# Kernel tuning notes

Measured on AMD Instinct MI355X. Metric: run time of the kernel, lower is better.

The kernel has to match this reference:

```python
import jax, jax.numpy as jnp
import numpy as np

DIM = 16
HEADS = 2
EPS = 1e-5


def _layer_norm(x, g, b):
    m = x.mean(-1, keepdims=True)
    v = ((x - m) ** 2).mean(-1, keepdims=True)
    return (x - m) * jax.lax.rsqrt(v + EPS) * g + b


def setup_inputs() -> dict:
    key = jax.random.key(0)
    ks = jax.random.split(key, 8)
    B, Lq, Lk, D = 4, 2048, 2048, DIM
    xavier = float(np.sqrt(6.0 / (D + D)))  # xavier_uniform bound for square Linear
    inp = {
        "query": jax.random.normal(ks[0], (B, Lq, D), jnp.float32),
        "key": jax.random.normal(ks[1], (B, Lk, D), jnp.float32),
        "value": jax.random.normal(ks[2], (B, Lk, D), jnp.float32),
        "w": jax.random.normal(ks[3], (B, HEADS, Lq, Lk), jnp.float32) * 0.1,
        "mask": jnp.zeros((B, HEADS, Lq, Lk), jnp.float32),
        # LayerNorm params (q, k, v)
        "ln_qg": jnp.ones((D,), jnp.float32), "ln_qb": jnp.zeros((D,), jnp.float32),
        "ln_kg": jnp.ones((D,), jnp.float32), "ln_kb": jnp.zeros((D,), jnp.float32),
        "ln_vg": jnp.ones((D,), jnp.float32), "ln_vb": jnp.zeros((D,), jnp.float32),
        # Linear projections, torch layout [out, in]
        "Wq": jax.random.uniform(ks[4], (D, D), jnp.float32, -xavier, xavier),
        "bq": jnp.zeros((D,), jnp.float32),
        "Wk": jax.random.uniform(ks[5], (D, D), jnp.float32, -xavier, xavier),
        "bk": jnp.zeros((D,), jnp.float32),
        "Wv": jax.random.uniform(ks[6], (D, D), jnp.float32, -xavier, xavier),
        "bv": jnp.zeros((D,), jnp.float32),
        "Wo": jax.random.normal(ks[7], (D, D), jnp.float32) * (1.0 / np.sqrt(D)),
        "bo": jnp.zeros((D,), jnp.float32),
    }
    return inp


def reference(query, key, value, w, mask,
              ln_qg, ln_qb, ln_kg, ln_kb, ln_vg, ln_vb,
              Wq, bq, Wk, bk, Wv, bv, Wo, bo):
    B, Lq, D = query.shape
    H = HEADS
    dh = D // H
    q = _layer_norm(query, ln_qg, ln_qb)
    k = _layer_norm(key, ln_kg, ln_kb)
    v = _layer_norm(value, ln_vg, ln_vb)
    q0 = q  # residual is post-LayerNorm query
    # torch Linear: x @ W.T + b ; split heads -> [B, H, L, dh]
    Q = (q @ Wq.T + bq).reshape(B, Lq, H, dh).transpose(0, 2, 1, 3)
    K = (k @ Wk.T + bk).reshape(B, -1, H, dh).transpose(0, 2, 1, 3)
    V = (v @ Wv.T + bv).reshape(B, -1, H, dh).transpose(0, 2, 1, 3)
    Q = Q / (dh ** 0.5)
    scores = jnp.einsum('bhqd,bhkd->bhqk', Q, K) + w
    scores = scores - scores.max(axis=-1, keepdims=True)
    scores = scores + mask
    attn = jax.nn.softmax(scores, axis=-1)  # dropout is identity in eval
    ctx = jnp.einsum('bhqk,bhkd->bhqd', attn, V)
    ctx = ctx.transpose(0, 2, 1, 3).reshape(B, Lq, D)
    out = ctx @ Wo.T + bo + q0
    return out, attn
```

## Files before the change

### kernel.cpp

```cpp
#include <hip/hip_runtime.h>
#include <math.h>

#define BATCH 4
#define LQ 2048
#define LK 2048
#define DIM 16
#define HEADS 2
#define DH 8
#define EPS 1e-5f

typedef float fvec4 __attribute__((ext_vector_type(4)));
typedef unsigned int uvec4 __attribute__((ext_vector_type(4)));
typedef unsigned int uvec2 __attribute__((ext_vector_type(2)));
typedef __fp16 hvec2 __attribute__((ext_vector_type(2)));

__device__ __forceinline__ hvec2 u2h(unsigned u) {
    union { unsigned u; hvec2 h; } c; c.u = u; return c.h;
}
__device__ __forceinline__ unsigned h2u(hvec2 h) {
    union { unsigned u; hvec2 h; } c; c.h = h; return c.u;
}

__global__ __launch_bounds__(256) void ln_proj3_kernel(
    const float* __restrict__ xq, const float* __restrict__ xk,
    const float* __restrict__ xv,
    const float* __restrict__ gq, const float* __restrict__ bq_ln,
    const float* __restrict__ gk, const float* __restrict__ bk_ln,
    const float* __restrict__ gv, const float* __restrict__ bv_ln,
    const float* __restrict__ Wq, const float* __restrict__ bq,
    const float* __restrict__ Wk, const float* __restrict__ bk,
    const float* __restrict__ Wv, const float* __restrict__ bv,
    float* __restrict__ Qb, unsigned* __restrict__ Kh,
    unsigned short* __restrict__ Vh, float* __restrict__ q0)
{
    const int gid = blockIdx.x * blockDim.x + threadIdx.x;
    const int which = gid >> 13;
    const int r     = gid & 8191;

    const float* x; const float* g; const float* bl;
    const float* W; const float* bb; float scale;
    if (which == 0)      { x = xq; g = gq; bl = bq_ln; W = Wq; bb = bq; scale = 0.35355339059327373f; }
    else if (which == 1) { x = xk; g = gk; bl = bk_ln; W = Wk; bb = bk; scale = 1.0f; }
    else                 { x = xv; g = gv; bl = bv_ln; W = Wv; bb = bv; scale = 1.0f; }

    float xv16[16];
    const float4* xp = (const float4*)(x + (size_t)r * 16);
#pragma unroll
    for (int i = 0; i < 4; ++i) {
        float4 t = xp[i];
        xv16[4*i+0] = t.x; xv16[4*i+1] = t.y; xv16[4*i+2] = t.z; xv16[4*i+3] = t.w;
    }
    float m = 0.f;
#pragma unroll
    for (int i = 0; i < 16; ++i) m += xv16[i];
    m *= (1.f / 16.f);
    float var = 0.f;
#pragma unroll
    for (int i = 0; i < 16; ++i) { float d = xv16[i] - m; var += d * d; }
    var *= (1.f / 16.f);
    float rs = rsqrtf(var + EPS);

    float xn[16];
#pragma unroll
    for (int i = 0; i < 16; ++i) xn[i] = (xv16[i] - m) * rs * g[i] + bl[i];

    if (which == 0) {
        float4* op = (float4*)(q0 + (size_t)r * 16);
#pragma unroll
        for (int i = 0; i < 4; ++i) {
            float4 t; t.x = xn[4*i+0]; t.y = xn[4*i+1]; t.z = xn[4*i+2]; t.w = xn[4*i+3];
            op[i] = t;
        }
    }

    float pr[16];
#pragma unroll
    for (int j = 0; j < 16; ++j) {
        float acc = bb[j];
#pragma unroll
        for (int i = 0; i < 16; ++i) acc += xn[i] * W[j * 16 + i];
        pr[j] = acc * scale;
    }

    const int b = r >> 11;
    const int l = r & 2047;
    if (which == 0) {
#pragma unroll
        for (int j = 0; j < 16; ++j) {
            int h = j >> 3, d = j & 7;
            Qb[((((size_t)b * HEADS + h) * 2048) + l) * DH + d] = pr[j];
        }
    } else if (which == 1) {
#pragma unroll
        for (int h = 0; h < 2; ++h) {
            unsigned* Kpan = Kh + ((size_t)(b * 2 + h)) * 8192;
#pragma unroll
            for (int p = 0; p < 4; ++p) {
                hvec2 hk = __builtin_amdgcn_cvt_pkrtz(pr[h * 8 + 2 * p], pr[h * 8 + 2 * p + 1]);
                Kpan[p * 2048 + l] = h2u(hk);
            }
        }
    } else {
#pragma unroll
        for (int h = 0; h < 2; ++h) {
            unsigned short* Vpan = Vh + ((size_t)(b * 2 + h)) * 16384;
#pragma unroll
            for (int d = 0; d < 8; ++d) {
                union { __fp16 h; unsigned short u; } cv;
                cv.h = (__fp16)pr[h * 8 + d];
                Vpan[d * 2048 + l] = cv.u;
            }
        }
    }
}

__device__ __forceinline__ float wave_sum(float v) {
#pragma unroll
    for (int off = 32; off > 0; off >>= 1) v += __shfl_xor(v, off);
    return v;
}

__global__ __launch_bounds__(256, 2) void attn_kernel(
    const float* __restrict__ Q,
    const unsigned* __restrict__ Kh,
    const unsigned* __restrict__ Vh,
    const float* __restrict__ w,
    const float* __restrict__ mask,
    float* __restrict__ attn_out,
    float* __restrict__ ctx)
{
    __shared__ unsigned Kp[4][2048];
    __shared__ unsigned Vp[8][1024];

    const int t    = threadIdx.x;
    const int lane = t & 63;
    const int wid  = t >> 6;
    const int gr   = (blockIdx.x << 2) + wid;
    const int bh   = gr >> 11;
    const int q    = gr & (LQ - 1);
    const int rowid= gr;
    const int h    = bh & (HEADS - 1);
    const int b    = bh >> 1;

    const unsigned* Kpan = Kh + (size_t)bh * 8192;
    const unsigned* Vpan = Vh + (size_t)bh * 8192;

    {
        const uvec4* Ksrc = (const uvec4*)Kpan;
        const uvec4* Vsrc = (const uvec4*)Vpan;
        uvec4* Kdst = (uvec4*)&Kp[0][0];
        uvec4* Vdst = (uvec4*)&Vp[0][0];
#pragma unroll
        for (int j = 0; j < 8; ++j) {
            Kdst[(j << 8) + t] = Ksrc[(j << 8) + t];
            Vdst[(j << 8) + t] = Vsrc[(j << 8) + t];
        }
    }

    const float* Qrow = Q + (size_t)rowid * DH;
    hvec2 qpk[4];
#pragma unroll
    for (int p = 0; p < 4; ++p) qpk[p] = __builtin_amdgcn_cvt_pkrtz(Qrow[2 * p], Qrow[2 * p + 1]);

    const float* wrow = w    + (size_t)rowid * LK;
    const float* mrow = mask + (size_t)rowid * LK;

    fvec4 wb[8], mb[8];
#pragma unroll
    for (int g = 0; g < 8; ++g) {
        const int col = (g << 8) + (lane << 2);
        wb[g] = __builtin_nontemporal_load((const fvec4*)(wrow + col));
        mb[g] = __builtin_nontemporal_load((const fvec4*)(mrow + col));
    }

    __syncthreads();

    unsigned epk[16];
    float sum = 0.f;
    float cd[8] = {0,0,0,0,0,0,0,0};

#pragma unroll
    for (int i = 0; i < 8; ++i) {
        const fvec4 wv = wb[i], mv = mb[i];
        const int cb = (i << 8) + (lane << 2);
        uvec4 kk0 = *(const uvec4*)&Kp[0][cb];
        uvec4 kk1 = *(const uvec4*)&Kp[1][cb];
        uvec4 kk2 = *(const uvec4*)&Kp[2][cb];
        uvec4 kk3 = *(const uvec4*)&Kp[3][cb];
        float e[4];
#pragma unroll
        for (int j = 0; j < 4; ++j) {
            float sj = wv[j] + mv[j] - 4.0f;
            sj = __builtin_amdgcn_fdot2(qpk[0], u2h(kk0[j]), sj, false);
            sj = __builtin_amdgcn_fdot2(qpk[1], u2h(kk1[j]), sj, false);
            sj = __builtin_amdgcn_fdot2(qpk[2], u2h(kk2[j]), sj, false);
            sj = __builtin_amdgcn_fdot2(qpk[3], u2h(kk3[j]), sj, false);
            e[j] = __expf(sj);
        }
        sum += (e[0] + e[1]) + (e[2] + e[3]);
        hvec2 e01 = __builtin_amdgcn_cvt_pkrtz(e[0], e[1]);
        hvec2 e23 = __builtin_amdgcn_cvt_pkrtz(e[2], e[3]);
        epk[2 * i]     = h2u(e01);
        epk[2 * i + 1] = h2u(e23);
        const int cp = cb >> 1;
#pragma unroll
        for (int d = 0; d < 8; ++d) {
            uvec2 vv = *(const uvec2*)&Vp[d][cp];
            cd[d] = __builtin_amdgcn_fdot2(e01, u2h(vv.x), cd[d], false);
            cd[d] = __builtin_amdgcn_fdot2(e23, u2h(vv.y), cd[d], false);
        }
    }

    sum = wave_sum(sum);
    const float inv = 1.f / sum;

    float* arow = attn_out + (size_t)rowid * LK;
#pragma unroll
    for (int g = 0; g < 8; ++g) {
        const int col = (g << 8) + (lane << 2);
        hvec2 e01 = u2h(epk[2 * g]), e23 = u2h(epk[2 * g + 1]);
        fvec4 o;
        o.x = (float)e01.x * inv; o.y = (float)e01.y * inv;
        o.z = (float)e23.x * inv; o.w = (float)e23.y * inv;
        __builtin_nontemporal_store(o, (fvec4*)(arow + col));
    }

#pragma unroll
    for (int d = 0; d < 8; ++d) cd[d] = wave_sum(cd[d]) * inv;
    if (lane == 0) {
        float* cp = ctx + ((((size_t)b * LQ + q) * HEADS) + h) * DH;
        fvec4 t0; t0.x = cd[0]; t0.y = cd[1]; t0.z = cd[2]; t0.w = cd[3];
        fvec4 t1; t1.x = cd[4]; t1.y = cd[5]; t1.z = cd[6]; t1.w = cd[7];
        ((fvec4*)cp)[0] = t0;
        ((fvec4*)cp)[1] = t1;
    }
}

__global__ __launch_bounds__(256) void out_kernel(
    const float* __restrict__ ctx,
    const float* __restrict__ Wo,
    const float* __restrict__ bo,
    const float* __restrict__ q0,
    float* __restrict__ out, int n)
{
    int gid = blockIdx.x * blockDim.x + threadIdx.x;
    if (gid >= n) return;
    int row = gid >> 4, j = gid & 15;
    const float* c = ctx + (size_t)row * 16;
    float acc = bo[j];
#pragma unroll
    for (int i = 0; i < 16; ++i) acc += c[i] * Wo[j * 16 + i];
    out[gid] = acc + q0[gid];
}

extern "C" void kernel_launch(void* const* d_in, const int* in_sizes, int n_in,
                              void* d_out, int out_size, void* d_ws, size_t ws_size,
                              hipStream_t stream) {
    const float* query = (const float*)d_in[0];
    const float* key_  = (const float*)d_in[1];
    const float* value = (const float*)d_in[2];
    const float* w     = (const float*)d_in[3];
    const float* mask  = (const float*)d_in[4];
    const float* ln_qg = (const float*)d_in[5];
    const float* ln_qb = (const float*)d_in[6];
    const float* ln_kg = (const float*)d_in[7];
    const float* ln_kb = (const float*)d_in[8];
    const float* ln_vg = (const float*)d_in[9];
    const float* ln_vb = (const float*)d_in[10];
    const float* Wq = (const float*)d_in[11];
    const float* bq = (const float*)d_in[12];
    const float* Wk = (const float*)d_in[13];
    const float* bk = (const float*)d_in[14];
    const float* Wv = (const float*)d_in[15];
    const float* bv = (const float*)d_in[16];
    const float* Wo = (const float*)d_in[17];
    const float* bo = (const float*)d_in[18];

    float* out  = (float*)d_out;
    float* attn = out + (size_t)BATCH * LQ * DIM;

    const size_t NE = (size_t)BATCH * LQ * DIM;
    float* ws  = (float*)d_ws;
    float* Qb  = ws;
    float* q0  = Qb + NE;
    float* ctx = q0 + NE;
    unsigned* Kh = (unsigned*)(ctx + NE);
    unsigned short* Vh16 = (unsigned short*)(Kh + 65536);
    unsigned* Vh = (unsigned*)Vh16;

    ln_proj3_kernel<<<(3 * 8192) / 256, 256, 0, stream>>>(
        query, key_, value,
        ln_qg, ln_qb, ln_kg, ln_kb, ln_vg, ln_vb,
        Wq, bq, Wk, bk, Wv, bv,
        Qb, Kh, Vh16, q0);

    attn_kernel<<<BATCH * HEADS * LQ / 4, 256, 0, stream>>>(
        Qb, Kh, Vh, w, mask, attn, ctx);

    out_kernel<<<((int)NE + 255) / 256, 256, 0, stream>>>(
        ctx, Wo, bo, q0, out, (int)NE);
}
```

Measured before the change: 80.91 us.

## Fuse output projection into attention via atomics and stage V from global

```diff
diff --git a/kernel.cpp b/kernel.cpp
--- a/kernel.cpp
+++ b/kernel.cpp
@@ -30,8 +30,10 @@
     const float* __restrict__ Wq, const float* __restrict__ bq,
     const float* __restrict__ Wk, const float* __restrict__ bk,
     const float* __restrict__ Wv, const float* __restrict__ bv,
+    const float* __restrict__ bo,
+    float* __restrict__ outbuf,
     float* __restrict__ Qb, unsigned* __restrict__ Kh,
-    unsigned short* __restrict__ Vh, float* __restrict__ q0)
+    unsigned short* __restrict__ Vh)
 {
     const int gid = blockIdx.x * blockDim.x + threadIdx.x;
     const int which = gid >> 13;
@@ -65,10 +67,12 @@
     for (int i = 0; i < 16; ++i) xn[i] = (xv16[i] - m) * rs * g[i] + bl[i];
 
     if (which == 0) {
-        float4* op = (float4*)(q0 + (size_t)r * 16);
+        float4* op = (float4*)(outbuf + (size_t)r * 16);
 #pragma unroll
         for (int i = 0; i < 4; ++i) {
-            float4 t; t.x = xn[4*i+0]; t.y = xn[4*i+1]; t.z = xn[4*i+2]; t.w = xn[4*i+3];
+            float4 t;
+            t.x = xn[4*i+0] + bo[4*i+0]; t.y = xn[4*i+1] + bo[4*i+1];
+            t.z = xn[4*i+2] + bo[4*i+2]; t.w = xn[4*i+3] + bo[4*i+3];
             op[i] = t;
         }
     }
@@ -120,17 +124,17 @@
     return v;
 }
 
-__global__ __launch_bounds__(256, 2) void attn_kernel(
+__global__ __launch_bounds__(256, 4) void attn_kernel(
     const float* __restrict__ Q,
     const unsigned* __restrict__ Kh,
     const unsigned* __restrict__ Vh,
     const float* __restrict__ w,
     const float* __restrict__ mask,
+    const float* __restrict__ Wo,
     float* __restrict__ attn_out,
-    float* __restrict__ ctx)
+    float* __restrict__ outbuf)
 {
     __shared__ unsigned Kp[4][2048];
-    __shared__ unsigned Vp[8][1024];
 
     const int t    = threadIdx.x;
     const int lane = t & 63;
@@ -145,16 +149,23 @@
     const unsigned* Kpan = Kh + (size_t)bh * 8192;
     const unsigned* Vpan = Vh + (size_t)bh * 8192;
 
+    const float* wrow = w    + (size_t)rowid * LK;
+    const float* mrow = mask + (size_t)rowid * LK;
+
+    fvec4 wb0[4], mb0[4];
+#pragma unroll
+    for (int g = 0; g < 4; ++g) {
+        const int col = (g << 8) + (lane << 2);
+        wb0[g] = __builtin_nontemporal_load((const fvec4*)(wrow + col));
+        mb0[g] = __builtin_nontemporal_load((const fvec4*)(mrow + col));
+    }
+
     {
         const uvec4* Ksrc = (const uvec4*)Kpan;
-        const uvec4* Vsrc = (const uvec4*)Vpan;
         uvec4* Kdst = (uvec4*)&Kp[0][0];
-        uvec4* Vdst = (uvec4*)&Vp[0][0];
-#pragma unroll
-        for (int j = 0; j < 8; ++j) {
+#pragma unroll
+        for (int j = 0; j < 8; ++j)
             Kdst[(j << 8) + t] = Ksrc[(j << 8) + t];
-            Vdst[(j << 8) + t] = Vsrc[(j << 8) + t];
-        }
     }
 
     const float* Qrow = Q + (size_t)rowid * DH;
@@ -162,27 +173,32 @@
 #pragma unroll
     for (int p = 0; p < 4; ++p) qpk[p] = __builtin_amdgcn_cvt_pkrtz(Qrow[2 * p], Qrow[2 * p + 1]);
 
-    const float* wrow = w    + (size_t)rowid * LK;
-    const float* mrow = mask + (size_t)rowid * LK;
-
-    fvec4 wb[8], mb[8];
-#pragma unroll
-    for (int g = 0; g < 8; ++g) {
-        const int col = (g << 8) + (lane << 2);
-        wb[g] = __builtin_nontemporal_load((const fvec4*)(wrow + col));
-        mb[g] = __builtin_nontemporal_load((const fvec4*)(mrow + col));
-    }
-
     __syncthreads();
+
+    fvec4 sb0[4];
+#pragma unroll
+    for (int g = 0; g < 4; ++g) sb0[g] = wb0[g] + mb0[g] - 4.0f;
+
+    fvec4 wb1[4], mb1[4];
+#pragma unroll
+    for (int g = 0; g < 4; ++g) {
+        const int col = ((g + 4) << 8) + (lane << 2);
+        wb1[g] = __builtin_nontemporal_load((const fvec4*)(wrow + col));
+        mb1[g] = __builtin_nontemporal_load((const fvec4*)(mrow + col));
+    }
+    __builtin_amdgcn_sched_barrier(0);
 
     unsigned epk[16];
     float sum = 0.f;
     float cd[8] = {0,0,0,0,0,0,0,0};
 
 #pragma unroll
-    for (int i = 0; i < 8; ++i) {
-        const fvec4 wv = wb[i], mv = mb[i];
+    for (int i = 0; i < 4; ++i) {
         const int cb = (i << 8) + (lane << 2);
+        const int cp = cb >> 1;
+        uvec2 vv[8];
+#pragma unroll
+        for (int d = 0; d < 8; ++d) vv[d] = *(const uvec2*)&Vpan[d * 1024 + cp];
         uvec4 kk0 = *(const uvec4*)&Kp[0][cb];
         uvec4 kk1 = *(const uvec4*)&Kp[1][cb];
         uvec4 kk2 = *(const uvec4*)&Kp[2][cb];
@@ -190,7 +206,7 @@
         float e[4];
 #pragma unroll
         for (int j = 0; j < 4; ++j) {
-            float sj = wv[j] + mv[j] - 4.0f;
+            float sj = sb0[i][j];
             sj = __builtin_amdgcn_fdot2(qpk[0], u2h(kk0[j]), sj, false);
             sj = __builtin_amdgcn_fdot2(qpk[1], u2h(kk1[j]), sj, false);
             sj = __builtin_amdgcn_fdot2(qpk[2], u2h(kk2[j]), sj, false);
@@ -202,12 +218,47 @@
         hvec2 e23 = __builtin_amdgcn_cvt_pkrtz(e[2], e[3]);
         epk[2 * i]     = h2u(e01);
         epk[2 * i + 1] = h2u(e23);
+#pragma unroll
+        for (int d = 0; d < 8; ++d) {
+            cd[d] = __builtin_amdgcn_fdot2(e01, u2h(vv[d].x), cd[d], false);
+            cd[d] = __builtin_amdgcn_fdot2(e23, u2h(vv[d].y), cd[d], false);
+        }
+    }
+
+    fvec4 sb1[4];
+#pragma unroll
+    for (int g = 0; g < 4; ++g) sb1[g] = wb1[g] + mb1[g] - 4.0f;
+
+#pragma unroll
+    for (int i = 0; i < 4; ++i) {
+        const int cb = ((i + 4) << 8) + (lane << 2);
         const int cp = cb >> 1;
+        uvec2 vv[8];
+#pragma unroll
+        for (int d = 0; d < 8; ++d) vv[d] = *(const uvec2*)&Vpan[d * 1024 + cp];
+        uvec4 kk0 = *(const uvec4*)&Kp[0][cb];
+        uvec4 kk1 = *(const uvec4*)&Kp[1][cb];
+        uvec4 kk2 = *(const uvec4*)&Kp[2][cb];
+        uvec4 kk3 = *(const uvec4*)&Kp[3][cb];
+        float e[4];
+#pragma unroll
+        for (int j = 0; j < 4; ++j) {
+            float sj = sb1[i][j];
+            sj = __builtin_amdgcn_fdot2(qpk[0], u2h(kk0[j]), sj, false);
+            sj = __builtin_amdgcn_fdot2(qpk[1], u2h(kk1[j]), sj, false);
+            sj = __builtin_amdgcn_fdot2(qpk[2], u2h(kk2[j]), sj, false);
+            sj = __builtin_amdgcn_fdot2(qpk[3], u2h(kk3[j]), sj, false);
+            e[j] = __expf(sj);
+        }
+        sum += (e[0] + e[1]) + (e[2] + e[3]);
+        hvec2 e01 = __builtin_amdgcn_cvt_pkrtz(e[0], e[1]);
+        hvec2 e23 = __builtin_amdgcn_cvt_pkrtz(e[2], e[3]);
+        epk[2 * (i + 4)]     = h2u(e01);
+        epk[2 * (i + 4) + 1] = h2u(e23);
 #pragma unroll
         for (int d = 0; d < 8; ++d) {
-            uvec2 vv = *(const uvec2*)&Vp[d][cp];
-            cd[d] = __builtin_amdgcn_fdot2(e01, u2h(vv.x), cd[d], false);
-            cd[d] = __builtin_amdgcn_fdot2(e23, u2h(vv.y), cd[d], false);
+            cd[d] = __builtin_amdgcn_fdot2(e01, u2h(vv[d].x), cd[d], false);
+            cd[d] = __builtin_amdgcn_fdot2(e23, u2h(vv[d].y), cd[d], false);
         }
     }
 
@@ -227,30 +278,13 @@
 
 #pragma unroll
     for (int d = 0; d < 8; ++d) cd[d] = wave_sum(cd[d]) * inv;
-    if (lane == 0) {
-        float* cp = ctx + ((((size_t)b * LQ + q) * HEADS) + h) * DH;
-        fvec4 t0; t0.x = cd[0]; t0.y = cd[1]; t0.z = cd[2]; t0.w = cd[3];
-        fvec4 t1; t1.x = cd[4]; t1.y = cd[5]; t1.z = cd[6]; t1.w = cd[7];
-        ((fvec4*)cp)[0] = t0;
-        ((fvec4*)cp)[1] = t1;
-    }
-}
-
-__global__ __launch_bounds__(256) void out_kernel(
-    const float* __restrict__ ctx,
-    const float* __restrict__ Wo,
-    const float* __restrict__ bo,
-    const float* __restrict__ q0,
-    float* __restrict__ out, int n)
-{
-    int gid = blockIdx.x * blockDim.x + threadIdx.x;
-    if (gid >= n) return;
-    int row = gid >> 4, j = gid & 15;
-    const float* c = ctx + (size_t)row * 16;
-    float acc = bo[j];
-#pragma unroll
-    for (int i = 0; i < 16; ++i) acc += c[i] * Wo[j * 16 + i];
-    out[gid] = acc + q0[gid];
+    if (lane < 16) {
+        const float* wo = Wo + lane * 16 + h * 8;
+        float acc = 0.f;
+#pragma unroll
+        for (int p = 0; p < 8; ++p) acc += cd[p] * wo[p];
+        atomicAdd(&outbuf[((size_t)(b * LQ + q)) * 16 + lane], acc);
+    }
 }
 
 extern "C" void kernel_launch(void* const* d_in, const int* in_sizes, int n_in,
@@ -282,9 +316,7 @@
     const size_t NE = (size_t)BATCH * LQ * DIM;
     float* ws  = (float*)d_ws;
     float* Qb  = ws;
-    float* q0  = Qb + NE;
-    float* ctx = q0 + NE;
-    unsigned* Kh = (unsigned*)(ctx + NE);
+    unsigned* Kh = (unsigned*)(Qb + NE);
     unsigned short* Vh16 = (unsigned short*)(Kh + 65536);
     unsigned* Vh = (unsigned*)Vh16;
 
@@ -292,11 +324,8 @@
         query, key_, value,
         ln_qg, ln_qb, ln_kg, ln_kb, ln_vg, ln_vb,
         Wq, bq, Wk, bk, Wv, bv,
-        Qb, Kh, Vh16, q0);
+        bo, out, Qb, Kh, Vh16);
 
     attn_kernel<<<BATCH * HEADS * LQ / 4, 256, 0, stream>>>(
-        Qb, Kh, Vh, w, mask, attn, ctx);
-
-    out_kernel<<<((int)NE + 255) / 256, 256, 0, stream>>>(
-        ctx, Wo, bo, q0, out, (int)NE);
-}
+        Qb, Kh, Vh, w, mask, Wo, attn, out);
+}
```

Result: slower. 96.28 us (+19.0%).

## Fuse output projection into attention kernel via atomic accumulation

Applied to the files above, without the earlier changes.

```diff
diff --git a/kernel.cpp b/kernel.cpp
--- a/kernel.cpp
+++ b/kernel.cpp
@@ -30,8 +30,10 @@
     const float* __restrict__ Wq, const float* __restrict__ bq,
     const float* __restrict__ Wk, const float* __restrict__ bk,
     const float* __restrict__ Wv, const float* __restrict__ bv,
+    const float* __restrict__ bo,
+    float* __restrict__ outbuf,
     float* __restrict__ Qb, unsigned* __restrict__ Kh,
-    unsigned short* __restrict__ Vh, float* __restrict__ q0)
+    unsigned short* __restrict__ Vh)
 {
     const int gid = blockIdx.x * blockDim.x + threadIdx.x;
     const int which = gid >> 13;
@@ -65,10 +67,12 @@
     for (int i = 0; i < 16; ++i) xn[i] = (xv16[i] - m) * rs * g[i] + bl[i];
 
     if (which == 0) {
-        float4* op = (float4*)(q0 + (size_t)r * 16);
+        float4* op = (float4*)(outbuf + (size_t)r * 16);
 #pragma unroll
         for (int i = 0; i < 4; ++i) {
-            float4 t; t.x = xn[4*i+0]; t.y = xn[4*i+1]; t.z = xn[4*i+2]; t.w = xn[4*i+3];
+            float4 t;
+            t.x = xn[4*i+0] + bo[4*i+0]; t.y = xn[4*i+1] + bo[4*i+1];
+            t.z = xn[4*i+2] + bo[4*i+2]; t.w = xn[4*i+3] + bo[4*i+3];
             op[i] = t;
         }
     }
@@ -126,8 +130,9 @@
     const unsigned* __restrict__ Vh,
     const float* __restrict__ w,
     const float* __restrict__ mask,
+    const float* __restrict__ Wo,
     float* __restrict__ attn_out,
-    float* __restrict__ ctx)
+    float* __restrict__ outbuf)
 {
     __shared__ unsigned Kp[4][2048];
     __shared__ unsigned Vp[8][1024];
@@ -227,30 +232,13 @@
 
 #pragma unroll
     for (int d = 0; d < 8; ++d) cd[d] = wave_sum(cd[d]) * inv;
-    if (lane == 0) {
-        float* cp = ctx + ((((size_t)b * LQ + q) * HEADS) + h) * DH;
-        fvec4 t0; t0.x = cd[0]; t0.y = cd[1]; t0.z = cd[2]; t0.w = cd[3];
-        fvec4 t1; t1.x = cd[4]; t1.y = cd[5]; t1.z = cd[6]; t1.w = cd[7];
-        ((fvec4*)cp)[0] = t0;
-        ((fvec4*)cp)[1] = t1;
-    }
-}
-
-__global__ __launch_bounds__(256) void out_kernel(
-    const float* __restrict__ ctx,
-    const float* __restrict__ Wo,
-    const float* __restrict__ bo,
-    const float* __restrict__ q0,
-    float* __restrict__ out, int n)
-{
-    int gid = blockIdx.x * blockDim.x + threadIdx.x;
-    if (gid >= n) return;
-    int row = gid >> 4, j = gid & 15;
-    const float* c = ctx + (size_t)row * 16;
-    float acc = bo[j];
-#pragma unroll
-    for (int i = 0; i < 16; ++i) acc += c[i] * Wo[j * 16 + i];
-    out[gid] = acc + q0[gid];
+    if (lane < 16) {
+        const float* wo = Wo + lane * 16 + h * 8;
+        float acc = 0.f;
+#pragma unroll
+        for (int p = 0; p < 8; ++p) acc += cd[p] * wo[p];
+        atomicAdd(&outbuf[((size_t)(b * LQ + q)) * 16 + lane], acc);
+    }
 }
 
 extern "C" void kernel_launch(void* const* d_in, const int* in_sizes, int n_in,
@@ -282,9 +270,7 @@
     const size_t NE = (size_t)BATCH * LQ * DIM;
     float* ws  = (float*)d_ws;
     float* Qb  = ws;
-    float* q0  = Qb + NE;
-    float* ctx = q0 + NE;
-    unsigned* Kh = (unsigned*)(ctx + NE);
+    unsigned* Kh = (unsigned*)(Qb + NE);
     unsigned short* Vh16 = (unsigned short*)(Kh + 65536);
     unsigned* Vh = (unsigned*)Vh16;
 
@@ -292,11 +278,8 @@
         query, key_, value,
         ln_qg, ln_qb, ln_kg, ln_kb, ln_vg, ln_vb,
         Wq, bq, Wk, bk, Wv, bv,
-        Qb, Kh, Vh16, q0);
+        bo, out, Qb, Kh, Vh16);
 
     attn_kernel<<<BATCH * HEADS * LQ / 4, 256, 0, stream>>>(
-        Qb, Kh, Vh, w, mask, attn, ctx);
-
-    out_kernel<<<((int)NE + 255) / 256, 256, 0, stream>>>(
-        ctx, Wo, bo, q0, out, (int)NE);
-}
+        Qb, Kh, Vh, w, mask, Wo, attn, out);
+}
```

New measurement: 80.99 us, median of 2. About the same (+0.1%).
